# Performance work log

Measured on AMD Instinct MI355X. Metric: run time of the kernel, lower is better.

The kernel has to match this reference:

```python
import math
import jax, jax.numpy as jnp
import numpy as np

NUM_HEADS = 16
EPS = 1e-12  # F.normalize default eps


def setup_inputs() -> dict:
    key = jax.random.key(0)
    ks = jax.random.split(key, 12)
    Bw, L, C = 1024, 144, 512
    num_win = 64
    s = 1.0 / math.sqrt(C)
    inp = {
        "x": jax.random.normal(ks[0], (Bw, L, C), dtype=jnp.float32),
        "mask": jax.random.normal(ks[1], (num_win, L, L), dtype=jnp.float32),
        "Wq": jax.random.normal(ks[2], (C, C), dtype=jnp.float32) * s,
        "bq": jnp.zeros((C,), dtype=jnp.float32),
        "Wk": jax.random.normal(ks[3], (C, C), dtype=jnp.float32) * s,
        "bk": jnp.zeros((C,), dtype=jnp.float32),
        "Wv": jax.random.normal(ks[4], (C, C), dtype=jnp.float32) * s,
        "bv": jnp.zeros((C,), dtype=jnp.float32),
        "Wp": jax.random.normal(ks[5], (C, C), dtype=jnp.float32) * s,
        "bp": jnp.zeros((C,), dtype=jnp.float32),
        "logit_scale": jnp.log(10.0 * jnp.ones((NUM_HEADS,), dtype=jnp.float32)),
    }
    return inp


def _l2norm(t):
    # matches F.normalize(dim=-1, eps=1e-12): x / max(||x||, eps)
    n = jnp.sqrt(jnp.sum(t * t, axis=-1, keepdims=True))
    return t / jnp.maximum(n, EPS)


def reference(x, mask, Wq, bq, Wk, bk, Wv, bv, Wp, bp, logit_scale):
    Bw, L, C = x.shape
    H = NUM_HEADS
    Dh = C // H
    num_win = mask.shape[0]

    def heads(t):  # (Bw, L, C) -> (Bw, H, L, Dh)
        return t.reshape(Bw, L, H, Dh).transpose(0, 2, 1, 3)

    q = heads(x @ Wq.T + bq)
    k = heads(x @ Wk.T + bk)
    v = heads(x @ Wv.T + bv)

    # cosine attention
    attn = jnp.einsum("bhld,bhmd->bhlm", _l2norm(q), _l2norm(k))
    scale = jnp.exp(jnp.minimum(logit_scale, math.log(1.0 / 0.01)))
    attn = attn * scale.reshape(1, H, 1, 1)

    # add shift mask: (Bw//nw, nw, H, L, L) + (1, nw, 1, L, L)
    attn = attn.reshape(Bw // num_win, num_win, H, L, L) + mask[None, :, None]
    attn = attn.reshape(Bw, H, L, L)

    attn = jax.nn.softmax(attn, axis=-1)
    out = jnp.einsum("bhlm,bhmd->bhld", attn, v)
    out = out.transpose(0, 2, 1, 3).reshape(Bw, L, C)
    return out @ Wp.T + bp
```

## Files before the change

### kernel.cpp

```cpp
#include <hip/hip_runtime.h>

typedef _Float16 half_t;
typedef __attribute__((ext_vector_type(8))) _Float16 half8;
typedef __attribute__((ext_vector_type(4))) _Float16 half4;
typedef __attribute__((ext_vector_type(4))) float f32x4;

#define GLD(gp, lp) \
  __builtin_amdgcn_global_load_lds((const __attribute__((address_space(1))) void*)(gp), \
                                   (__attribute__((address_space(3))) void*)(lp), 16, 0, 0)

__global__ __launch_bounds__(256) void cvt_kernel(const float* __restrict__ src,
                                                  half_t* __restrict__ dst, int n4) {
  int i = blockIdx.x * 256 + threadIdx.x;
  int stride = gridDim.x * 256;
  for (; i < n4; i += stride) {
    f32x4 v = *((const f32x4*)src + i);
    half4 o;
    o[0] = (half_t)v[0]; o[1] = (half_t)v[1];
    o[2] = (half_t)v[2]; o[3] = (half_t)v[3];
    *((half4*)dst + i) = o;
  }
}

__global__ __launch_bounds__(256) void qkv_gemm(
    const half_t* __restrict__ xh,
    const half_t* __restrict__ wq, const half_t* __restrict__ wk, const half_t* __restrict__ wv,
    const float* __restrict__ bq, const float* __restrict__ bk, const float* __restrict__ bv,
    const float* __restrict__ logit_scale,
    half_t* __restrict__ qout, half_t* __restrict__ kout, half_t* __restrict__ vout) {
  __shared__ alignas(16) half_t As[128 * 32];
  __shared__ alignas(16) half_t Bs[128 * 32];

  int bid = blockIdx.x;
  int mtile = bid / 12, nsub = bid % 12;
  int mat = nsub >> 2;
  int n0 = (nsub & 3) << 7;
  long m0 = (long)mtile << 7;
  const half_t* W    = (mat == 0) ? wq : (mat == 1) ? wk : wv;
  const float*  bias = (mat == 0) ? bq : (mat == 1) ? bk : bv;
  half_t*       out  = (mat == 0) ? qout : (mat == 1) ? kout : vout;

  int tid = threadIdx.x, lane = tid & 63, wid = tid >> 6;
  int quad = lane >> 4, c = lane & 15;
  int wm = (wid & 1) << 6, wn = (wid >> 1) << 6;

  f32x4 acc[4][4] = {};

  const half_t* Abase = xh + m0 * 512;
  const half_t* Bbase = W + (long)n0 * 512;
  int r_lo = lane >> 2;
  int cp   = (lane & 3) << 3;

  for (int kk = 0; kk < 512; kk += 32) {
#pragma unroll
    for (int ci = 0; ci < 2; ci++) {
      int ch = wid + ci * 4;
      int row = (ch << 4) + r_lo;
      GLD(Abase + (long)row * 512 + kk + cp, As + (ch << 9));
      GLD(Bbase + (long)row * 512 + kk + cp, Bs + (ch << 9));
    }
    __syncthreads();
    half8 af[4], bf[4];
#pragma unroll
    for (int mi = 0; mi < 4; mi++)
      af[mi] = *(const half8*)(As + ((wm + (mi << 4) + c) << 5) + (quad << 3));
#pragma unroll
    for (int ni = 0; ni < 4; ni++)
      bf[ni] = *(const half8*)(Bs + ((wn + (ni << 4) + c) << 5) + (quad << 3));
#pragma unroll
    for (int mi = 0; mi < 4; mi++)
#pragma unroll
      for (int ni = 0; ni < 4; ni++)
        acc[mi][ni] = __builtin_amdgcn_mfma_f32_16x16x32_f16(af[mi], bf[ni], acc[mi][ni], 0, 0, 0);
    __syncthreads();
  }

#pragma unroll
  for (int mi = 0; mi < 4; mi++) {
#pragma unroll
    for (int hh = 0; hh < 2; hh++) {
      f32x4 a0 = acc[mi][2 * hh], a1 = acc[mi][2 * hh + 1];
      int col0 = n0 + wn + (hh << 5) + c;
      float b0 = bias[col0], b1 = bias[col0 + 16];
#pragma unroll
      for (int r = 0; r < 4; r++) { a0[r] += b0; a1[r] += b1; }
      if (mat != 2) {
        float sc = 1.f;
        if (mat == 0) {
          int hidx = (n0 + wn + (hh << 5)) >> 5;
          sc = __expf(fminf(logit_scale[hidx], 4.60517018598809f));
        }
        float ss[4];
#pragma unroll
        for (int r = 0; r < 4; r++) ss[r] = a0[r] * a0[r] + a1[r] * a1[r];
#pragma unroll
        for (int d = 1; d < 16; d <<= 1)
#pragma unroll
          for (int r = 0; r < 4; r++) ss[r] += __shfl_xor(ss[r], d);
#pragma unroll
        for (int r = 0; r < 4; r++) {
          float inv = sc / fmaxf(sqrtf(ss[r]), 1e-12f);
          a0[r] *= inv; a1[r] *= inv;
        }
      }
      long grow = m0 + wm + (mi << 4) + (quad << 2);
#pragma unroll
      for (int r = 0; r < 4; r++) {
        out[(grow + r) * 512 + col0]      = (half_t)a0[r];
        out[(grow + r) * 512 + col0 + 16] = (half_t)a1[r];
      }
    }
  }
}

__global__ __launch_bounds__(576) void attn_kernel(
    const half_t* __restrict__ qh, const half_t* __restrict__ kh, const half_t* __restrict__ vh,
    const float* __restrict__ mask, half_t* __restrict__ Oh) {
  __shared__ alignas(16) half_t Pl[144 * 176];
  __shared__ alignas(16) half_t Vt[32 * 176];
  int b = blockIdx.x, h = blockIdx.y;
  int win = b & 63;
  int tid = threadIdx.x, lane = tid & 63, w = tid >> 6;
  int quad = lane >> 4, c = lane & 15;

  const half_t* vbase = vh + ((long)b * 144) * 512 + h * 32;
#pragma unroll
  for (int t = 0; t < 8; t++) {
    int i = tid + t * 576;
    int l = i >> 5, d = i & 31;
    Vt[d * 176 + l] = vbase[(long)l * 512 + d];
  }
  if (tid < 512) { int d = tid >> 4, l = 144 + (tid & 15); Vt[d * 176 + l] = (half_t)0.f; }
  __syncthreads();

  const half_t* qbase = qh + ((long)b * 144) * 512 + h * 32;
  const half_t* kbase = kh + ((long)b * 144) * 512 + h * 32;
  half8 aq = *(const half8*)(qbase + (long)(w * 16 + c) * 512 + quad * 8);
  f32x4 s[9];
#pragma unroll
  for (int nt = 0; nt < 9; nt++) {
    half8 bk = *(const half8*)(kbase + (long)(nt * 16 + c) * 512 + quad * 8);
    f32x4 z = {0.f, 0.f, 0.f, 0.f};
    s[nt] = __builtin_amdgcn_mfma_f32_16x16x32_f16(aq, bk, z, 0, 0, 0);
  }

  const float* mbase = mask + ((long)win * 144 + w * 16 + quad * 4) * 144 + c;
  float mx[4] = {-1e30f, -1e30f, -1e30f, -1e30f};
#pragma unroll
  for (int nt = 0; nt < 9; nt++)
#pragma unroll
    for (int r = 0; r < 4; r++) {
      s[nt][r] += mbase[r * 144 + nt * 16];
      mx[r] = fmaxf(mx[r], s[nt][r]);
    }
#pragma unroll
  for (int d = 1; d < 16; d <<= 1)
#pragma unroll
    for (int r = 0; r < 4; r++) mx[r] = fmaxf(mx[r], __shfl_xor(mx[r], d));

  float sum[4] = {0.f, 0.f, 0.f, 0.f};
#pragma unroll
  for (int nt = 0; nt < 9; nt++)
#pragma unroll
    for (int r = 0; r < 4; r++) {
      float p = __expf(s[nt][r] - mx[r]);
      s[nt][r] = p; sum[r] += p;
    }
#pragma unroll
  for (int d = 1; d < 16; d <<= 1)
#pragma unroll
    for (int r = 0; r < 4; r++) sum[r] += __shfl_xor(sum[r], d);

  int prow = w * 16 + quad * 4;
#pragma unroll
  for (int r = 0; r < 4; r++) {
#pragma unroll
    for (int nt = 0; nt < 9; nt++)
      Pl[(prow + r) * 176 + nt * 16 + c] = (half_t)s[nt][r];
    Pl[(prow + r) * 176 + 144 + c] = (half_t)0.f;
  }

  f32x4 o0 = {0.f, 0.f, 0.f, 0.f}, o1 = {0.f, 0.f, 0.f, 0.f};
#pragma unroll
  for (int ks = 0; ks < 5; ks++) {
    half8 ap = *(const half8*)(Pl + (w * 16 + c) * 176 + ks * 32 + quad * 8);
    half8 b0 = *(const half8*)(Vt + c * 176 + ks * 32 + quad * 8);
    half8 b1 = *(const half8*)(Vt + (16 + c) * 176 + ks * 32 + quad * 8);
    o0 = __builtin_amdgcn_mfma_f32_16x16x32_f16(ap, b0, o0, 0, 0, 0);
    o1 = __builtin_amdgcn_mfma_f32_16x16x32_f16(ap, b1, o1, 0, 0, 0);
  }

  half_t* obase = Oh + ((long)b * 144) * 512 + h * 32;
#pragma unroll
  for (int r = 0; r < 4; r++) {
    float rs = 1.f / sum[r];
    obase[(long)(prow + r) * 512 + c]      = (half_t)(o0[r] * rs);
    obase[(long)(prow + r) * 512 + 16 + c] = (half_t)(o1[r] * rs);
  }
}

__global__ __launch_bounds__(256) void out_gemm(
    const half_t* __restrict__ Ah, const half_t* __restrict__ W,
    const float* __restrict__ bias, float* __restrict__ y) {
  __shared__ alignas(16) half_t As[128 * 32];
  __shared__ alignas(16) half_t Bs[128 * 32];
  int bid = blockIdx.x;
  long m0 = (long)(bid >> 2) << 7;
  int n0 = (bid & 3) << 7;
  int tid = threadIdx.x, lane = tid & 63, wid = tid >> 6;
  int quad = lane >> 4, c = lane & 15;
  int wm = (wid & 1) << 6, wn = (wid >> 1) << 6;
  f32x4 acc[4][4] = {};
  const half_t* Abase = Ah + m0 * 512;
  const half_t* Bbase = W + (long)n0 * 512;
  int r_lo = lane >> 2, cp = (lane & 3) << 3;

  for (int kk = 0; kk < 512; kk += 32) {
#pragma unroll
    for (int ci = 0; ci < 2; ci++) {
      int ch = wid + ci * 4;
      int row = (ch << 4) + r_lo;
      GLD(Abase + (long)row * 512 + kk + cp, As + (ch << 9));
      GLD(Bbase + (long)row * 512 + kk + cp, Bs + (ch << 9));
    }
    __syncthreads();
    half8 af[4], bf[4];
#pragma unroll
    for (int mi = 0; mi < 4; mi++)
      af[mi] = *(const half8*)(As + ((wm + (mi << 4) + c) << 5) + (quad << 3));
#pragma unroll
    for (int ni = 0; ni < 4; ni++)
      bf[ni] = *(const half8*)(Bs + ((wn + (ni << 4) + c) << 5) + (quad << 3));
#pragma unroll
    for (int mi = 0; mi < 4; mi++)
#pragma unroll
      for (int ni = 0; ni < 4; ni++)
        acc[mi][ni] = __builtin_amdgcn_mfma_f32_16x16x32_f16(af[mi], bf[ni], acc[mi][ni], 0, 0, 0);
    __syncthreads();
  }
#pragma unroll
  for (int mi = 0; mi < 4; mi++)
#pragma unroll
    for (int ni = 0; ni < 4; ni++) {
      int col = n0 + wn + (ni << 4) + c;
      float bv_ = bias[col];
      long grow = m0 + wm + (mi << 4) + (quad << 2);
#pragma unroll
      for (int r = 0; r < 4; r++)
        y[(grow + r) * 512 + col] = acc[mi][ni][r] + bv_;
    }
}

extern "C" void kernel_launch(void* const* d_in, const int* in_sizes, int n_in,
                              void* d_out, int out_size, void* d_ws, size_t ws_size,
                              hipStream_t stream) {
  const float* x    = (const float*)d_in[0];
  const float* mask = (const float*)d_in[1];
  const float* Wq   = (const float*)d_in[2];
  const float* bq   = (const float*)d_in[3];
  const float* Wk   = (const float*)d_in[4];
  const float* bk   = (const float*)d_in[5];
  const float* Wv   = (const float*)d_in[6];
  const float* bv   = (const float*)d_in[7];
  const float* Wp   = (const float*)d_in[8];
  const float* bp   = (const float*)d_in[9];
  const float* ls   = (const float*)d_in[10];

  const long MT = 147456L * 512;
  half_t* xh  = (half_t*)d_ws;
  half_t* vh  = xh + MT;
  half_t* Oh  = vh + MT;
  half_t* wqh = Oh + MT;
  half_t* wkh = wqh + 262144;
  half_t* wvh = wkh + 262144;
  half_t* wph = wvh + 262144;
  half_t* qh  = (half_t*)d_out;
  half_t* kh  = qh + MT;
  float*  y   = (float*)d_out;

  cvt_kernel<<<73728, 256, 0, stream>>>(x, xh, (int)(MT / 4));
  cvt_kernel<<<256, 256, 0, stream>>>(Wq, wqh, 65536);
  cvt_kernel<<<256, 256, 0, stream>>>(Wk, wkh, 65536);
  cvt_kernel<<<256, 256, 0, stream>>>(Wv, wvh, 65536);
  cvt_kernel<<<256, 256, 0, stream>>>(Wp, wph, 65536);
  qkv_gemm<<<13824, 256, 0, stream>>>(xh, wqh, wkh, wvh, bq, bk, bv, ls, qh, kh, vh);
  attn_kernel<<<dim3(1024, 16), 576, 0, stream>>>(qh, kh, vh, mask, Oh);
  out_gemm<<<4608, 256, 0, stream>>>(Oh, wph, bp, y);
}
```

Measured before the change: 1.463 ms.

## Double-buffer LDS tiles in QKV and output GEMMs and remap block order

Both GEMM kernels now keep two LDS buffers and issue the global-to-LDS loads for the next K slice right after the barrier, so loads overlap the MFMA work on the current slice. The trailing barrier is dropped, leaving one barrier per iteration. Block indices are also remapped with an 8-way stride, meant to spread neighbouring blocks across XCDs and improve L2 locality for the shared row tiles. LDS use per block doubles, which may reduce occupancy. The single barrier relies on the async global_load_lds writes having completed before the next barrier, which is not explicitly waited on.

```diff
diff --git a/kernel.cpp b/kernel.cpp
--- a/kernel.cpp
+++ b/kernel.cpp
@@ -28,10 +28,12 @@
     const float* __restrict__ bq, const float* __restrict__ bk, const float* __restrict__ bv,
     const float* __restrict__ logit_scale,
     half_t* __restrict__ qout, half_t* __restrict__ kout, half_t* __restrict__ vout) {
-  __shared__ alignas(16) half_t As[128 * 32];
-  __shared__ alignas(16) half_t Bs[128 * 32];
+  __shared__ alignas(16) half_t As[2 * 128 * 32];
+  __shared__ alignas(16) half_t Bs[2 * 128 * 32];
 
   int bid = blockIdx.x;
+  bid = (bid & 7) * 1728 + (bid >> 3);
+
   int mtile = bid / 12, nsub = bid % 12;
   int mat = nsub >> 2;
   int n0 = (nsub & 3) << 7;
@@ -51,28 +53,39 @@
   int r_lo = lane >> 2;
   int cp   = (lane & 3) << 3;
 
+#define STAGE_T(buf, kkv)                                                        \
+  {                                                                              \
+    _Pragma("unroll")                                                            \
+    for (int ci = 0; ci < 2; ci++) {                                             \
+      int ch = wid + ci * 4;                                                     \
+      int row = (ch << 4) + r_lo;                                                \
+      GLD(Abase + (long)row * 512 + (kkv) + cp, As + (buf) * 4096 + (ch << 9));  \
+      GLD(Bbase + (long)row * 512 + (kkv) + cp, Bs + (buf) * 4096 + (ch << 9));  \
+    }                                                                            \
+  }
+
+  STAGE_T(0, 0);
+  int cur = 0;
+
   for (int kk = 0; kk < 512; kk += 32) {
-#pragma unroll
-    for (int ci = 0; ci < 2; ci++) {
-      int ch = wid + ci * 4;
-      int row = (ch << 4) + r_lo;
-      GLD(Abase + (long)row * 512 + kk + cp, As + (ch << 9));
-      GLD(Bbase + (long)row * 512 + kk + cp, Bs + (ch << 9));
-    }
     __syncthreads();
+    if (kk < 480) STAGE_T(cur ^ 1, kk + 32);
+
+    const half_t* Ab = As + cur * 4096;
+    const half_t* Bb = Bs + cur * 4096;
     half8 af[4], bf[4];
 #pragma unroll
     for (int mi = 0; mi < 4; mi++)
-      af[mi] = *(const half8*)(As + ((wm + (mi << 4) + c) << 5) + (quad << 3));
+      af[mi] = *(const half8*)(Ab + ((wm + (mi << 4) + c) << 5) + (quad << 3));
 #pragma unroll
     for (int ni = 0; ni < 4; ni++)
-      bf[ni] = *(const half8*)(Bs + ((wn + (ni << 4) + c) << 5) + (quad << 3));
+      bf[ni] = *(const half8*)(Bb + ((wn + (ni << 4) + c) << 5) + (quad << 3));
 #pragma unroll
     for (int mi = 0; mi < 4; mi++)
 #pragma unroll
       for (int ni = 0; ni < 4; ni++)
         acc[mi][ni] = __builtin_amdgcn_mfma_f32_16x16x32_f16(af[mi], bf[ni], acc[mi][ni], 0, 0, 0);
-    __syncthreads();
+    cur ^= 1;
   }
 
 #pragma unroll
@@ -111,6 +124,7 @@
       }
     }
   }
+#undef STAGE_T
 }
 
 __global__ __launch_bounds__(576) void attn_kernel(
@@ -202,9 +216,12 @@
 __global__ __launch_bounds__(256) void out_gemm(
     const half_t* __restrict__ Ah, const half_t* __restrict__ W,
     const float* __restrict__ bias, float* __restrict__ y) {
-  __shared__ alignas(16) half_t As[128 * 32];
-  __shared__ alignas(16) half_t Bs[128 * 32];
+  __shared__ alignas(16) half_t As[2 * 128 * 32];
+  __shared__ alignas(16) half_t Bs[2 * 128 * 32];
+
   int bid = blockIdx.x;
+  bid = (bid & 7) * 576 + (bid >> 3);
+
   long m0 = (long)(bid >> 2) << 7;
   int n0 = (bid & 3) << 7;
   int tid = threadIdx.x, lane = tid & 63, wid = tid >> 6;
@@ -215,29 +232,41 @@
   const half_t* Bbase = W + (long)n0 * 512;
   int r_lo = lane >> 2, cp = (lane & 3) << 3;
 
+#define STAGE_T(buf, kkv)                                                        \
+  {                                                                              \
+    _Pragma("unroll")                                                            \
+    for (int ci = 0; ci < 2; ci++) {                                             \
+      int ch = wid + ci * 4;                                                     \
+      int row = (ch << 4) + r_lo;                                                \
+      GLD(Abase + (long)row * 512 + (kkv) + cp, As + (buf) * 4096 + (ch << 9));  \
+      GLD(Bbase + (long)row * 512 + (kkv) + cp, Bs + (buf) * 4096 + (ch << 9));  \
+    }                                                                            \
+  }
+
+  STAGE_T(0, 0);
+  int cur = 0;
+
   for (int kk = 0; kk < 512; kk += 32) {
-#pragma unroll
-    for (int ci = 0; ci < 2; ci++) {
-      int ch = wid + ci * 4;
-      int row = (ch << 4) + r_lo;
-      GLD(Abase + (long)row * 512 + kk + cp, As + (ch << 9));
-      GLD(Bbase + (long)row * 512 + kk + cp, Bs + (ch << 9));
-    }
     __syncthreads();
+    if (kk < 480) STAGE_T(cur ^ 1, kk + 32);
+
+    const half_t* Ab = As + cur * 4096;
+    const half_t* Bb = Bs + cur * 4096;
     half8 af[4], bf[4];
 #pragma unroll
     for (int mi = 0; mi < 4; mi++)
-      af[mi] = *(const half8*)(As + ((wm + (mi << 4) + c) << 5) + (quad << 3));
+      af[mi] = *(const half8*)(Ab + ((wm + (mi << 4) + c) << 5) + (quad << 3));
 #pragma unroll
     for (int ni = 0; ni < 4; ni++)
-      bf[ni] = *(const half8*)(Bs + ((wn + (ni << 4) + c) << 5) + (quad << 3));
+      bf[ni] = *(const half8*)(Bb + ((wn + (ni << 4) + c) << 5) + (quad << 3));
 #pragma unroll
     for (int mi = 0; mi < 4; mi++)
 #pragma unroll
       for (int ni = 0; ni < 4; ni++)
         acc[mi][ni] = __builtin_amdgcn_mfma_f32_16x16x32_f16(af[mi], bf[ni], acc[mi][ni], 0, 0, 0);
-    __syncthreads();
-  }
+    cur ^= 1;
+  }
+
 #pragma unroll
   for (int mi = 0; mi < 4; mi++)
 #pragma unroll
@@ -249,6 +278,7 @@
       for (int r = 0; r < 4; r++)
         y[(grow + r) * 512 + col] = acc[mi][ni][r] + bv_;
     }
+#undef STAGE_T
 }
 
 extern "C" void kernel_launch(void* const* d_in, const int* in_sizes, int n_in,
```

Result: faster. 1.410 ms (-3.6%).
